# Kernel tuning notes

Hardware: AMD Instinct MI355X
Metric: run time of the kernel (lower is better)

The kernel has to match this reference:

```python
import jax, jax.numpy as jnp
import numpy as np
from jax import lax

B, T = 512, 64
IN, H, V1, P = 256, 512, 101, 8  # input_size, rnn_size, vocab_size+1, max_param
CLS, REG = 512, 512


def setup_inputs() -> dict:
    key = jax.random.key(0)
    ks = jax.random.split(key, 20)
    u = lambda k, s: jax.random.uniform(k, s, jnp.float32, -0.1, 0.1)
    sh = 1.0 / np.sqrt(H)
    ul = lambda k, s: jax.random.uniform(k, s, jnp.float32, -sh, sh)
    return {
        "x": jax.random.normal(ks[0], (B, IN), jnp.float32),
        "y": jax.random.randint(ks[1], (B, T), 0, V1),
        "embed": u(ks[2], (V1, IN)),
        "w_ih0": ul(ks[3], (4 * H, IN)),
        "w_hh0": ul(ks[4], (4 * H, H)),
        "w_ih1": ul(ks[5], (4 * H, H)),
        "w_hh1": ul(ks[6], (4 * H, H)),
        "l1w": u(ks[7], (CLS, H)), "l1b": jnp.zeros((CLS,), jnp.float32),
        "l2w": u(ks[8], (V1, CLS)), "l2b": jnp.zeros((V1,), jnp.float32),
        "r1w": u(ks[9], (REG, H)), "r1b": jnp.zeros((REG,), jnp.float32),
        "r2w": u(ks[10], (V1 * P, V1 + REG)), "r2b": jnp.zeros((V1 * P,), jnp.float32),
    }


def _cell(xi, h, c, wih, whh):
    g = xi @ wih.T + h @ whh.T          # [B, 4H], gate order i,f,g,o (no bias)
    i, f, gg, o = jnp.split(g, 4, axis=-1)
    c = jax.nn.sigmoid(f) * c + jax.nn.sigmoid(i) * jnp.tanh(gg)
    h = jax.nn.sigmoid(o) * jnp.tanh(c)
    return h, c


def reference(x, y, embed, w_ih0, w_hh0, w_ih1, w_hh1,
              l1w, l1b, l2w, l2b, r1w, r1b, r2w, r2b):
    # teacher forcing (sample_prob=0): step-0 input is x, step-i input is embed(y[:, i-1])
    emb = embed[y[:, :-1]]                                  # [B, T-1, IN]
    xt = jnp.concatenate([x[None], jnp.transpose(emb, (1, 0, 2))], axis=0)  # [T, B, IN]

    z = jnp.zeros((x.shape[0], H), x.dtype)

    def step(carry, xi):
        h0, c0, h1, c1 = carry
        h0, c0 = _cell(xi, h0, c0, w_ih0, w_hh0)
        h1, c1 = _cell(h0, h1, c1, w_ih1, w_hh1)
        return (h0, c0, h1, c1), h1

    _, outs = lax.scan(step, (z, z, z, z), xt)              # [T, B, H]

    feat2 = jax.nn.relu(outs @ l1w.T + l1b) @ l2w.T + l2b   # [T, B, V1]
    pgm_score = jax.nn.log_softmax(feat2, axis=-1)
    trans_prob = lax.stop_gradient(jax.nn.softmax(feat2, axis=-1))
    pf1 = jax.nn.relu(outs @ r1w.T + r1b)                   # [T, B, REG]
    ps = (jnp.concatenate([trans_prob, pf1], axis=-1) @ r2w.T + r2b)
    ps = ps.reshape(T, -1, V1, P)                           # [T, B, V1, P]
    idx = y.T                                               # [T, B]
    param = ps[jnp.arange(T)[:, None], jnp.arange(x.shape[0])[None, :], idx]  # [T, B, P]
    return (jnp.transpose(pgm_score, (1, 0, 2)),            # [B, T, V1]
            jnp.transpose(param, (1, 0, 2)))                # [B, T, P]
```

## Files before the change

kernel.cpp:

```cpp
#include <hip/hip_runtime.h>
#include <stdint.h>

typedef unsigned short u16;
typedef short bf16x8 __attribute__((ext_vector_type(8)));
typedef float f32x4 __attribute__((ext_vector_type(4)));
typedef int i32x4 __attribute__((ext_vector_type(4)));

#define DEV static __device__ __forceinline__

constexpr int B_ = 512, T_ = 64, IN_ = 256, H_ = 512, V1_ = 101, P_ = 8, G4_ = 2048;
constexpr int EXR = 613;
constexpr int M_  = T_ * B_;

DEV float b2f(u16 u) { union { uint32_t i; float f; } v; v.i = ((uint32_t)u) << 16; return v.f; }
DEV u16 f2b(float f) {
  union { float f; uint32_t i; } v; v.f = f;
  uint32_t i = v.i;
  return (u16)((i + 0x7fffu + ((i >> 16) & 1u)) >> 16);
}
DEV float sigf(float x) { return 1.f / (1.f + __expf(-x)); }
DEV float tanh_(float x) {
  float c = fminf(fmaxf(x, -15.f), 15.f);
  float e = __expf(2.f * c);
  return (e - 1.f) / (e + 1.f);
}
DEV bf16x8 ld8(const u16* p) { return *reinterpret_cast<const bf16x8*>(p); }
DEV f32x4 mfma16(bf16x8 a, bf16x8 b, f32x4 c) {
  return __builtin_amdgcn_mfma_f32_16x16x32_bf16(a, b, c, 0, 0, 0);
}

struct CvtArgs {
  const float* src[9];
  u16* dst[9];
  int pre[10];
};

__global__ __launch_bounds__(256) void k_cvtall(CvtArgs a) {
  int gid = blockIdx.x * 256 + threadIdx.x;
  if (gid >= a.pre[9]) return;
  int s = 0;
#pragma unroll
  for (int i = 1; i < 9; ++i) s += (gid >= a.pre[i]);
  const int local = gid - a.pre[s];
  const float4 v = reinterpret_cast<const float4*>(a.src[s])[local];
  ushort4 o;
  o.x = f2b(v.x); o.y = f2b(v.y); o.z = f2b(v.z); o.w = f2b(v.w);
  reinterpret_cast<ushort4*>(a.dst[s])[local] = o;
}

__global__ __launch_bounds__(256) void k_precomp(const u16* __restrict__ ex_src,
                                                 const u16* __restrict__ wih0b,
                                                 float* __restrict__ EX0) {
  const int lane = threadIdx.x & 63;
  const int wv = threadIdx.x >> 6;
  const int m0 = blockIdx.x * 64 + wv * 16;
  const int n0 = blockIdx.y * 64;
  const int lr = lane & 15;
  const int lk = (lane >> 4) * 8;

  const int arow = m0 + lr;
  const bool valid = arow < EXR;

  f32x4 acc[4] = {};
  for (int k0 = 0; k0 < IN_; k0 += 32) {
    bf16x8 a = {};
    if (valid) a = ld8(ex_src + (size_t)arow * IN_ + k0 + lk);
#pragma unroll
    for (int c = 0; c < 4; ++c) {
      bf16x8 b = ld8(wih0b + (size_t)(n0 + c * 16 + lr) * IN_ + k0 + lk);
      acc[c] = mfma16(a, b, acc[c]);
    }
  }
  const int rb = (lane >> 4) * 4;
#pragma unroll
  for (int c = 0; c < 4; ++c)
#pragma unroll
    for (int r = 0; r < 4; ++r) {
      int row = m0 + rb + r;
      int col = n0 + c * 16 + (lane & 15);
      if (row < EXR) EX0[(size_t)row * G4_ + col] = acc[c][r];
    }
}

__global__ __launch_bounds__(256, 1) void k_scan(
    const u16* __restrict__ whh0, const u16* __restrict__ wih1, const u16* __restrict__ whh1,
    const float* __restrict__ EX0, const int* __restrict__ y,
    u16* h0buf, u16* h1buf, unsigned* flags ) {
  __shared__ u16 h0s[16 * 512];
  __shared__ u16 h1s[16 * 512];
  __shared__ u16 stg[16][64];
  const size_t BH = (size_t)B_ * H_;
  const int tid = threadIdx.x;
  const int lane = tid & 63;
  const int wv = tid >> 6;
  const int isL1 = blockIdx.x >> 8;
  const int bm = (blockIdx.x >> 3) & 31;
  const int bj = blockIdx.x & 7;
  const int lr = lane & 15;
  const int lk = (lane >> 4) * 8;
  const int col = bj * 64 + wv * 16 + lr;
  const int rb = (lane >> 4) * 4;
  const int lcol = wv * 16 + lr;

  const u16* wpa[4]; const u16* wpb[4];
#pragma unroll
  for (int g = 0; g < 4; ++g) {
    wpa[g] = (isL1 ? wih1 : whh0) + (size_t)(g * H_ + col) * H_ + lk;
    wpb[g] = (isL1 ? whh1 : whh0) + (size_t)(g * H_ + col) * H_ + lk;
  }
  f32x4 cst = {};
  unsigned* gf = flags + bm * 16;
  const int npoll = isL1 ? 16 : 8;

  for (int k = 0; k < T_; ++k) {
    if (wv == 0 && (k > 0 || isL1)) {
      const unsigned thr = (lane < 8) ? (unsigned)(isL1 ? k + 1 : k)
                                      : ((lane < 16 && isL1) ? (unsigned)k : 0u);
      for (;;) {
        unsigned v = 0xffffffffu;
        if (lane < npoll)
          v = __hip_atomic_load(&gf[lane], __ATOMIC_RELAXED, __HIP_MEMORY_SCOPE_AGENT);
        if (__all(v >= thr)) break;
        __builtin_amdgcn_s_sleep(1);
      }
    }
    __syncthreads();

    {
      const u16* h0g = h0buf + (size_t)(k + isL1) * BH + (size_t)(bm * 16) * H_;
#pragma unroll
      for (int rr = 0; rr < 4; ++rr) {
        const int idx = rr * 256 + tid;
        const int row = idx >> 6, cc = idx & 63;
        i32x4 d = *(const i32x4*)(h0g + (size_t)row * H_ + cc * 8);
        *(i32x4*)((char*)h0s + row * 1024 + ((cc * 16) ^ ((row & 7) << 4))) = d;
      }
      if (isL1) {
        const u16* h1g = h1buf + (size_t)k * BH + (size_t)(bm * 16) * H_;
#pragma unroll
        for (int rr = 0; rr < 4; ++rr) {
          const int idx = rr * 256 + tid;
          const int row = idx >> 6, cc = idx & 63;
          i32x4 d = *(const i32x4*)(h1g + (size_t)row * H_ + cc * 8);
          *(i32x4*)((char*)h1s + row * 1024 + ((cc * 16) ^ ((row & 7) << 4))) = d;
        }
      }
    }
    __syncthreads();

    if (!isL1) {
      f32x4 acc[4] = {};
#pragma unroll
      for (int i = 0; i < 16; ++i) {
        bf16x8 a0 = *(const bf16x8*)((const char*)h0s + lr * 1024 + (((i * 32 + lk) * 2) ^ ((lr & 7) << 4)));
#pragma unroll
        for (int g = 0; g < 4; ++g) acc[g] = mfma16(a0, ld8(wpa[g] + i * 32), acc[g]);
      }
#pragma unroll
      for (int r = 0; r < 4; ++r) {
        const int row = bm * 16 + rb + r;
        const int srow = (k == 0) ? (V1_ + row) : y[row * T_ + k - 1];
        const float* bp = EX0 + (size_t)srow * G4_ + col;
        float iv = acc[0][r] + bp[0], fv = acc[1][r] + bp[H_];
        float gv = acc[2][r] + bp[2 * H_], ov = acc[3][r] + bp[3 * H_];
        float cn = sigf(fv) * cst[r] + sigf(iv) * tanh_(gv);
        cst[r] = cn;
        stg[rb + r][lcol] = f2b(sigf(ov) * tanh_(cn));
      }
    } else {
      f32x4 acc[4] = {};
#pragma unroll
      for (int i = 0; i < 16; ++i) {
        const int so = ((i * 32 + lk) * 2) ^ ((lr & 7) << 4);
        bf16x8 a0 = *(const bf16x8*)((const char*)h0s + lr * 1024 + so);
        bf16x8 a1 = *(const bf16x8*)((const char*)h1s + lr * 1024 + so);
#pragma unroll
        for (int g = 0; g < 4; ++g) {
          acc[g] = mfma16(a0, ld8(wpa[g] + i * 32), acc[g]);
          acc[g] = mfma16(a1, ld8(wpb[g] + i * 32), acc[g]);
        }
      }
#pragma unroll
      for (int r = 0; r < 4; ++r) {
        float cn = sigf(acc[1][r]) * cst[r] + sigf(acc[0][r]) * tanh_(acc[2][r]);
        cst[r] = cn;
        stg[rb + r][lcol] = f2b(sigf(acc[3][r]) * tanh_(cn));
      }
    }
    __syncthreads();

    if (tid < 128) {
      const int lrow = tid >> 3, c8 = (tid & 7) * 8;
      i32x4 d = *(const i32x4*)&stg[lrow][c8];
      u16* base = isL1 ? h1buf : h0buf;
      u16* gp = base + (size_t)(k + 1) * BH + (size_t)(bm * 16 + lrow) * H_ + bj * 64 + c8;
      asm volatile("global_store_dwordx4 %0, %1, off sc0 sc1" :: "v"(gp), "v"(d) : "memory");
    }
    asm volatile("s_waitcnt vmcnt(0)" ::: "memory");
    __syncthreads();
    if (tid == 0)
      __hip_atomic_store(&gf[isL1 * 8 + bj], (unsigned)(k + 1),
                         __ATOMIC_RELAXED, __HIP_MEMORY_SCOPE_AGENT);
  }
}

__global__ __launch_bounds__(256) void k_fused1(const u16* __restrict__ outs,
                                                const u16* __restrict__ l1w, const float* __restrict__ l1b,
                                                const u16* __restrict__ r1w, const float* __restrict__ r1b,
                                                u16* __restrict__ feat1, u16* __restrict__ pf1) {
  const int lane = threadIdx.x & 63;
  const int wv = threadIdx.x >> 6;
  const int lr = lane & 15;
  const int lk = (lane >> 4) * 8;
  const int ar = blockIdx.x * 64 + wv * 16 + lr;
  const int rb = (lane >> 4) * 4;
  const int row0 = blockIdx.x * 64 + wv * 16 + rb;

  bf16x8 a[16];
  {
    const u16* ap = outs + (size_t)ar * H_ + lk;
#pragma unroll
    for (int i = 0; i < 16; ++i) a[i] = ld8(ap + i * 32);
  }
  for (int w = 0; w < 2; ++w) {
    const u16* W = w ? r1w : l1w;
    const float* bias = w ? r1b : l1b;
    u16* dst = w ? pf1 : feat1;
    for (int nc = 0; nc < 4; ++nc) {
      f32x4 acc[8] = {};
#pragma unroll
      for (int i = 0; i < 16; ++i)
#pragma unroll
        for (int n = 0; n < 8; ++n)
          acc[n] = mfma16(a[i], ld8(W + (size_t)(nc * 128 + n * 16 + lr) * H_ + i * 32 + lk), acc[n]);
#pragma unroll
      for (int n = 0; n < 8; ++n) {
        const int colc = nc * 128 + n * 16 + lr;
        const float bv = bias[colc];
#pragma unroll
        for (int r = 0; r < 4; ++r)
          dst[(size_t)(row0 + r) * H_ + colc] = f2b(fmaxf(acc[n][r] + bv, 0.f));
      }
    }
  }
}

__global__ __launch_bounds__(256) void k_fused2(const u16* __restrict__ feat1,
                                                const u16* __restrict__ l2w, const float* __restrict__ l2b,
                                                const u16* __restrict__ pf1,
                                                const float* __restrict__ r2w, const float* __restrict__ r2b,
                                                const int* __restrict__ y,
                                                float* __restrict__ pgm, float* __restrict__ par) {
  __shared__ float trans[64][104];
  const int lane = threadIdx.x & 63;
  const int wv = threadIdx.x >> 6;
  const int lr = lane & 15;
  const int lk = (lane >> 4) * 8;
  const int ar = blockIdx.x * 64 + wv * 16 + lr;
  const int rb = (lane >> 4) * 4;

  f32x4 acc[7] = {};
  {
    const u16* ap = feat1 + (size_t)ar * H_ + lk;
#pragma unroll
    for (int i = 0; i < 16; ++i) {
      bf16x8 av = ld8(ap + i * 32);
#pragma unroll
      for (int c = 0; c < 7; ++c) {
        const int n = c * 16 + lr;
        bf16x8 b = {};
        if (n < V1_) b = ld8(l2w + (size_t)n * H_ + i * 32 + lk);
        acc[c] = mfma16(av, b, acc[c]);
      }
    }
  }
#pragma unroll
  for (int r = 0; r < 4; ++r) {
    float v[7];
    float mx = -1e30f;
#pragma unroll
    for (int c = 0; c < 7; ++c) {
      const int colc = c * 16 + lr;
      v[c] = (colc < V1_) ? acc[c][r] + l2b[colc] : -1e30f;
      mx = fmaxf(mx, v[c]);
    }
#pragma unroll
    for (int o = 1; o < 16; o <<= 1) mx = fmaxf(mx, __shfl_xor(mx, o, 64));
    float e[7], s = 0.f;
#pragma unroll
    for (int c = 0; c < 7; ++c) { e[c] = (c * 16 + lr < V1_) ? __expf(v[c] - mx) : 0.f; s += e[c]; }
#pragma unroll
    for (int o = 1; o < 16; o <<= 1) s += __shfl_xor(s, o, 64);
    const float lz = __logf(s), inv = 1.f / s;
    const int m = blockIdx.x * 64 + wv * 16 + rb + r;
    const int t = m >> 9, bb = m & 511;
    float* po = pgm + ((size_t)bb * T_ + t) * V1_;
#pragma unroll
    for (int c = 0; c < 7; ++c) {
      const int colc = c * 16 + lr;
      if (colc < V1_) { po[colc] = v[c] - mx - lz; trans[wv * 16 + rb + r][colc] = e[c] * inv; }
    }
  }
  __syncthreads();
  for (int rr = 0; rr < 16; ++rr) {
    const int m = blockIdx.x * 64 + wv * 16 + rr;
    const int t = m >> 9, bb = m & 511;
    const int idx = y[bb * T_ + t];
    const float* wb = r2w + (size_t)idx * P_ * 613;
    float a8[P_] = {};
    for (int kk = lane; kk < 613; kk += 64) {
      float xv = (kk < V1_) ? trans[wv * 16 + rr][kk] : b2f(pf1[(size_t)m * H_ + kk - V1_]);
#pragma unroll
      for (int p = 0; p < P_; ++p) a8[p] += xv * wb[(size_t)p * 613 + kk];
    }
#pragma unroll
    for (int p = 0; p < P_; ++p)
#pragma unroll
      for (int o = 1; o < 64; o <<= 1) a8[p] += __shfl_xor(a8[p], o, 64);
    if (lane < P_) par[((size_t)bb * T_ + t) * P_ + lane] = a8[lane] + r2b[idx * P_ + lane];
  }
}

extern "C" void kernel_launch(void* const* d_in, const int* in_sizes, int n_in,
                              void* d_out, int out_size, void* d_ws, size_t ws_size,
                              hipStream_t stream) {
  (void)in_sizes; (void)n_in; (void)out_size; (void)ws_size;
  const float* x     = (const float*)d_in[0];
  const int*   y     = (const int*)d_in[1];
  const float* embed = (const float*)d_in[2];
  const float* wih0  = (const float*)d_in[3];
  const float* whh0  = (const float*)d_in[4];
  const float* wih1  = (const float*)d_in[5];
  const float* whh1  = (const float*)d_in[6];
  const float* l1w   = (const float*)d_in[7];
  const float* l1b   = (const float*)d_in[8];
  const float* l2w   = (const float*)d_in[9];
  const float* l2b   = (const float*)d_in[10];
  const float* r1w   = (const float*)d_in[11];
  const float* r1b   = (const float*)d_in[12];
  const float* r2w   = (const float*)d_in[13];
  const float* r2b   = (const float*)d_in[14];

  float* out_pgm = (float*)d_out;
  float* out_par = out_pgm + (size_t)B_ * T_ * V1_;

  char* ws = (char*)d_ws;
  size_t off = 0;
  auto alloc = [&](size_t bytes) { void* p = ws + off; off += (bytes + 255) & ~(size_t)255; return p; };

  const size_t BH2 = (size_t)B_ * H_ * 2;

  unsigned* flags = (unsigned*)alloc(32 * 16 * 4);
  u16* h0buf  = (u16*)alloc((size_t)(T_ + 1) * BH2);
  u16* h1buf  = (u16*)alloc((size_t)(T_ + 1) * BH2);

  float* EX0   = (float*)alloc((size_t)EXR * G4_ * 4);
  u16* ex_src  = (u16*)alloc((size_t)EXR * IN_ * 2);
  u16* wih0b   = (u16*)alloc((size_t)4 * H_ * IN_ * 2);
  u16* whh0b   = (u16*)alloc((size_t)4 * H_ * H_ * 2);
  u16* wih1b   = (u16*)alloc((size_t)4 * H_ * H_ * 2);
  u16* whh1b   = (u16*)alloc((size_t)4 * H_ * H_ * 2);
  u16* l1wb    = (u16*)alloc((size_t)H_ * H_ * 2);
  u16* r1wb    = (u16*)alloc((size_t)H_ * H_ * 2);
  u16* l2wb    = (u16*)alloc((size_t)V1_ * H_ * 2);
  u16* feat1   = (u16*)alloc((size_t)M_ * H_ * 2);
  u16* pf1     = (u16*)alloc((size_t)M_ * H_ * 2);

  (void)hipMemsetAsync(flags, 0, 32 * 16 * 4 + BH2, stream);
  (void)hipMemsetAsync(h1buf, 0, BH2, stream);

  CvtArgs ca;
  const float* srcs[9] = {embed, x, wih0, whh0, wih1, whh1, l1w, r1w, l2w};
  u16* dsts[9] = {ex_src, ex_src + (size_t)V1_ * IN_, wih0b, whh0b, wih1b, whh1b, l1wb, r1wb, l2wb};
  int ns[9] = {V1_ * IN_, B_ * IN_, 4 * H_ * IN_, 4 * H_ * H_, 4 * H_ * H_, 4 * H_ * H_,
               H_ * H_, H_ * H_, V1_ * H_};
  int acc4 = 0;
  for (int i = 0; i < 9; ++i) {
    ca.src[i] = srcs[i]; ca.dst[i] = dsts[i]; ca.pre[i] = acc4; acc4 += ns[i] / 4;
  }
  ca.pre[9] = acc4;
  k_cvtall<<<(acc4 + 255) / 256, 256, 0, stream>>>(ca);

  k_precomp<<<dim3(10, 32), 256, 0, stream>>>(ex_src, wih0b, EX0);

  k_scan<<<512, 256, 0, stream>>>(whh0b, wih1b, whh1b, EX0, y, h0buf, h1buf, flags);

  u16* outs = h1buf + (size_t)B_ * H_;
  k_fused1<<<512, 256, 0, stream>>>(outs, l1wb, l1b, r1wb, r1b, feat1, pf1);
  k_fused2<<<512, 256, 0, stream>>>(feat1, l2wb, l2b, pf1, r2w, r2b, y, out_pgm, out_par);
}
```

Before: 2.089 ms.

## Repartition persistent LSTM scan to 256 blocks of 512 threads, store EX0 in bf16

```diff
diff --git a/kernel.cpp b/kernel.cpp
--- a/kernel.cpp
+++ b/kernel.cpp
@@ -50,7 +50,7 @@
 
 __global__ __launch_bounds__(256) void k_precomp(const u16* __restrict__ ex_src,
                                                  const u16* __restrict__ wih0b,
-                                                 float* __restrict__ EX0) {
+                                                 u16* __restrict__ EX0) {
   const int lane = threadIdx.x & 63;
   const int wv = threadIdx.x >> 6;
   const int m0 = blockIdx.x * 64 + wv * 16;
@@ -78,29 +78,36 @@
     for (int r = 0; r < 4; ++r) {
       int row = m0 + rb + r;
       int col = n0 + c * 16 + (lane & 15);
-      if (row < EXR) EX0[(size_t)row * G4_ + col] = acc[c][r];
-    }
-}
-
-__global__ __launch_bounds__(256, 1) void k_scan(
+      if (row < EXR) EX0[(size_t)row * G4_ + col] = f2b(acc[c][r]);
+    }
+}
+
+__global__ __launch_bounds__(512, 1) void k_scan(
     const u16* __restrict__ whh0, const u16* __restrict__ wih1, const u16* __restrict__ whh1,
-    const float* __restrict__ EX0, const int* __restrict__ y,
+    const u16* __restrict__ EX0, const int* __restrict__ y,
     u16* h0buf, u16* h1buf, unsigned* flags ) {
-  __shared__ u16 h0s[16 * 512];
-  __shared__ u16 h1s[16 * 512];
-  __shared__ u16 stg[16][64];
+  __shared__ u16 h0s[32 * 512];
+  __shared__ u16 h1s[32 * 512];
+  __shared__ u16 stg[2048];
   const size_t BH = (size_t)B_ * H_;
   const int tid = threadIdx.x;
   const int lane = tid & 63;
   const int wv = tid >> 6;
-  const int isL1 = blockIdx.x >> 8;
-  const int bm = (blockIdx.x >> 3) & 31;
-  const int bj = blockIdx.x & 7;
+  const int x_ = blockIdx.x & 7;
+  const int n  = blockIdx.x >> 3;
+  const bool isL1 = x_ >= 4;
+  const int xr = x_ & 3;
+  const int Rb = xr * 128;
   const int lr = lane & 15;
   const int lk = (lane >> 4) * 8;
-  const int col = bj * 64 + wv * 16 + lr;
   const int rb = (lane >> 4) * 4;
-  const int lcol = wv * 16 + lr;
+
+  const int rm = n & 7, cs = n >> 3;
+  const int rm2 = n & 3, cw = n >> 2;
+
+  int col, arow0;
+  if (!isL1) { col = cs * 128 + wv * 16 + lr; arow0 = 0; }
+  else       { col = cw * 64 + (wv >> 1) * 16 + lr; arow0 = (wv & 1) * 16; }
 
   const u16* wpa[4]; const u16* wpb[4];
 #pragma unroll
@@ -109,17 +116,23 @@
     wpb[g] = (isL1 ? whh1 : whh0) + (size_t)(g * H_ + col) * H_ + lk;
   }
   f32x4 cst = {};
-  unsigned* gf = flags + bm * 16;
-  const int npoll = isL1 ? 16 : 8;
+  unsigned* f0g = flags + xr * 32 + (isL1 ? rm2 * 8 : rm * 4);
+  unsigned* f1g = flags + 128 + xr * 32 + rm2 * 8;
+
+  const int row0base = isL1 ? (Rb + rm2 * 32) : (Rb + rm * 16);
+  const int nrows = isL1 ? 32 : 16;
 
   for (int k = 0; k < T_; ++k) {
     if (wv == 0 && (k > 0 || isL1)) {
-      const unsigned thr = (lane < 8) ? (unsigned)(isL1 ? k + 1 : k)
-                                      : ((lane < 16 && isL1) ? (unsigned)k : 0u);
+      unsigned thr = 0; const unsigned* ap = nullptr;
+      if (!isL1) { if (lane < 4) { ap = f0g + lane; thr = (unsigned)k; } }
+      else {
+        if (lane < 8)       { ap = f0g + lane;     thr = (unsigned)(k + 1); }
+        else if (lane < 16) { ap = f1g + lane - 8; thr = (unsigned)k; }
+      }
       for (;;) {
         unsigned v = 0xffffffffu;
-        if (lane < npoll)
-          v = __hip_atomic_load(&gf[lane], __ATOMIC_RELAXED, __HIP_MEMORY_SCOPE_AGENT);
+        if (ap) v = __hip_atomic_load(ap, __ATOMIC_RELAXED, __HIP_MEMORY_SCOPE_AGENT);
         if (__all(v >= thr)) break;
         __builtin_amdgcn_s_sleep(1);
       }
@@ -127,19 +140,16 @@
     __syncthreads();
 
     {
-      const u16* h0g = h0buf + (size_t)(k + isL1) * BH + (size_t)(bm * 16) * H_;
-#pragma unroll
-      for (int rr = 0; rr < 4; ++rr) {
-        const int idx = rr * 256 + tid;
+      const u16* h0g = h0buf + (size_t)(k + (isL1 ? 1 : 0)) * BH + (size_t)row0base * H_;
+      const int nch = nrows * 64;
+      for (int idx = tid; idx < nch; idx += 512) {
         const int row = idx >> 6, cc = idx & 63;
         i32x4 d = *(const i32x4*)(h0g + (size_t)row * H_ + cc * 8);
         *(i32x4*)((char*)h0s + row * 1024 + ((cc * 16) ^ ((row & 7) << 4))) = d;
       }
       if (isL1) {
-        const u16* h1g = h1buf + (size_t)k * BH + (size_t)(bm * 16) * H_;
-#pragma unroll
-        for (int rr = 0; rr < 4; ++rr) {
-          const int idx = rr * 256 + tid;
+        const u16* h1g = h1buf + (size_t)k * BH + (size_t)row0base * H_;
+        for (int idx = tid; idx < nch; idx += 512) {
           const int row = idx >> 6, cc = idx & 63;
           i32x4 d = *(const i32x4*)(h1g + (size_t)row * H_ + cc * 8);
           *(i32x4*)((char*)h1s + row * 1024 + ((cc * 16) ^ ((row & 7) << 4))) = d;
@@ -156,51 +166,60 @@
 #pragma unroll
         for (int g = 0; g < 4; ++g) acc[g] = mfma16(a0, ld8(wpa[g] + i * 32), acc[g]);
       }
+      const int lcol = wv * 16 + lr;
 #pragma unroll
       for (int r = 0; r < 4; ++r) {
-        const int row = bm * 16 + rb + r;
+        const int row = row0base + rb + r;
         const int srow = (k == 0) ? (V1_ + row) : y[row * T_ + k - 1];
-        const float* bp = EX0 + (size_t)srow * G4_ + col;
-        float iv = acc[0][r] + bp[0], fv = acc[1][r] + bp[H_];
-        float gv = acc[2][r] + bp[2 * H_], ov = acc[3][r] + bp[3 * H_];
+        const u16* bp = EX0 + (size_t)srow * G4_ + col;
+        float iv = acc[0][r] + b2f(bp[0]), fv = acc[1][r] + b2f(bp[H_]);
+        float gv = acc[2][r] + b2f(bp[2 * H_]), ov = acc[3][r] + b2f(bp[3 * H_]);
         float cn = sigf(fv) * cst[r] + sigf(iv) * tanh_(gv);
         cst[r] = cn;
-        stg[rb + r][lcol] = f2b(sigf(ov) * tanh_(cn));
+        stg[(rb + r) * 128 + lcol] = f2b(sigf(ov) * tanh_(cn));
       }
     } else {
       f32x4 acc[4] = {};
 #pragma unroll
       for (int i = 0; i < 16; ++i) {
-        const int so = ((i * 32 + lk) * 2) ^ ((lr & 7) << 4);
-        bf16x8 a0 = *(const bf16x8*)((const char*)h0s + lr * 1024 + so);
-        bf16x8 a1 = *(const bf16x8*)((const char*)h1s + lr * 1024 + so);
+        const int so = ((i * 32 + lk) * 2) ^ (((arow0 + lr) & 7) << 4);
+        bf16x8 a0 = *(const bf16x8*)((const char*)h0s + (arow0 + lr) * 1024 + so);
+        bf16x8 a1 = *(const bf16x8*)((const char*)h1s + (arow0 + lr) * 1024 + so);
 #pragma unroll
         for (int g = 0; g < 4; ++g) {
           acc[g] = mfma16(a0, ld8(wpa[g] + i * 32), acc[g]);
           acc[g] = mfma16(a1, ld8(wpb[g] + i * 32), acc[g]);
         }
       }
+      const int lcol = (wv >> 1) * 16 + lr;
 #pragma unroll
       for (int r = 0; r < 4; ++r) {
         float cn = sigf(acc[1][r]) * cst[r] + sigf(acc[0][r]) * tanh_(acc[2][r]);
         cst[r] = cn;
-        stg[rb + r][lcol] = f2b(sigf(acc[3][r]) * tanh_(cn));
+        stg[(arow0 + rb + r) * 64 + lcol] = f2b(sigf(acc[3][r]) * tanh_(cn));
       }
     }
     __syncthreads();
 
-    if (tid < 128) {
-      const int lrow = tid >> 3, c8 = (tid & 7) * 8;
-      i32x4 d = *(const i32x4*)&stg[lrow][c8];
-      u16* base = isL1 ? h1buf : h0buf;
-      u16* gp = base + (size_t)(k + 1) * BH + (size_t)(bm * 16 + lrow) * H_ + bj * 64 + c8;
-      asm volatile("global_store_dwordx4 %0, %1, off sc0 sc1" :: "v"(gp), "v"(d) : "memory");
+    if (tid < 256) {
+      if (!isL1) {
+        const int lrow = tid >> 4, c8 = (tid & 15) * 8;
+        i32x4 d = *(const i32x4*)&stg[lrow * 128 + c8];
+        u16* gp = h0buf + (size_t)(k + 1) * BH + (size_t)(row0base + lrow) * H_ + cs * 128 + c8;
+        asm volatile("global_store_dwordx4 %0, %1, off sc0 sc1" :: "v"(gp), "v"(d) : "memory");
+      } else {
+        const int lrow = tid >> 3, c8 = (tid & 7) * 8;
+        i32x4 d = *(const i32x4*)&stg[lrow * 64 + c8];
+        u16* gp = h1buf + (size_t)(k + 1) * BH + (size_t)(row0base + lrow) * H_ + cw * 64 + c8;
+        asm volatile("global_store_dwordx4 %0, %1, off sc0 sc1" :: "v"(gp), "v"(d) : "memory");
+      }
     }
     asm volatile("s_waitcnt vmcnt(0)" ::: "memory");
     __syncthreads();
-    if (tid == 0)
-      __hip_atomic_store(&gf[isL1 * 8 + bj], (unsigned)(k + 1),
-                         __ATOMIC_RELAXED, __HIP_MEMORY_SCOPE_AGENT);
+    if (tid == 0) {
+      unsigned* fa = isL1 ? &f1g[cw] : &f0g[cs];
+      __hip_atomic_store(fa, (unsigned)(k + 1), __ATOMIC_RELAXED, __HIP_MEMORY_SCOPE_AGENT);
+    }
   }
 }
 
@@ -231,15 +250,15 @@
 #pragma unroll
       for (int i = 0; i < 16; ++i)
 #pragma unroll
-        for (int n = 0; n < 8; ++n)
-          acc[n] = mfma16(a[i], ld8(W + (size_t)(nc * 128 + n * 16 + lr) * H_ + i * 32 + lk), acc[n]);
-#pragma unroll
-      for (int n = 0; n < 8; ++n) {
-        const int colc = nc * 128 + n * 16 + lr;
+        for (int nn = 0; nn < 8; ++nn)
+          acc[nn] = mfma16(a[i], ld8(W + (size_t)(nc * 128 + nn * 16 + lr) * H_ + i * 32 + lk), acc[nn]);
+#pragma unroll
+      for (int nn = 0; nn < 8; ++nn) {
+        const int colc = nc * 128 + nn * 16 + lr;
         const float bv = bias[colc];
 #pragma unroll
         for (int r = 0; r < 4; ++r)
-          dst[(size_t)(row0 + r) * H_ + colc] = f2b(fmaxf(acc[n][r] + bv, 0.f));
+          dst[(size_t)(row0 + r) * H_ + colc] = f2b(fmaxf(acc[nn][r] + bv, 0.f));
       }
     }
   }
@@ -267,9 +286,9 @@
       bf16x8 av = ld8(ap + i * 32);
 #pragma unroll
       for (int c = 0; c < 7; ++c) {
-        const int n = c * 16 + lr;
+        const int nn = c * 16 + lr;
         bf16x8 b = {};
-        if (n < V1_) b = ld8(l2w + (size_t)n * H_ + i * 32 + lk);
+        if (nn < V1_) b = ld8(l2w + (size_t)nn * H_ + i * 32 + lk);
         acc[c] = mfma16(av, b, acc[c]);
       }
     }
@@ -350,11 +369,11 @@
 
   const size_t BH2 = (size_t)B_ * H_ * 2;
 
-  unsigned* flags = (unsigned*)alloc(32 * 16 * 4);
+  unsigned* flags = (unsigned*)alloc(256 * 4);
   u16* h0buf  = (u16*)alloc((size_t)(T_ + 1) * BH2);
   u16* h1buf  = (u16*)alloc((size_t)(T_ + 1) * BH2);
 
-  float* EX0   = (float*)alloc((size_t)EXR * G4_ * 4);
+  u16* EX0b    = (u16*)alloc((size_t)EXR * G4_ * 2);
   u16* ex_src  = (u16*)alloc((size_t)EXR * IN_ * 2);
   u16* wih0b   = (u16*)alloc((size_t)4 * H_ * IN_ * 2);
   u16* whh0b   = (u16*)alloc((size_t)4 * H_ * H_ * 2);
@@ -366,7 +385,7 @@
   u16* feat1   = (u16*)alloc((size_t)M_ * H_ * 2);
   u16* pf1     = (u16*)alloc((size_t)M_ * H_ * 2);
 
-  (void)hipMemsetAsync(flags, 0, 32 * 16 * 4 + BH2, stream);
+  (void)hipMemsetAsync(flags, 0, 256 * 4 + BH2, stream);
   (void)hipMemsetAsync(h1buf, 0, BH2, stream);
 
   CvtArgs ca;
@@ -381,9 +400,9 @@
   ca.pre[9] = acc4;
   k_cvtall<<<(acc4 + 255) / 256, 256, 0, stream>>>(ca);
 
-  k_precomp<<<dim3(10, 32), 256, 0, stream>>>(ex_src, wih0b, EX0);
-
-  k_scan<<<512, 256, 0, stream>>>(whh0b, wih1b, whh1b, EX0, y, h0buf, h1buf, flags);
+  k_precomp<<<dim3(10, 32), 256, 0, stream>>>(ex_src, wih0b, EX0b);
+
+  k_scan<<<256, 512, 0, stream>>>(whh0b, wih1b, whh1b, EX0b, y, h0buf, h1buf, flags);
 
   u16* outs = h1buf + (size_t)B_ * H_;
   k_fused1<<<512, 256, 0, stream>>>(outs, l1wb, l1b, r1wb, r1b, feat1, pf1);
```

Measured after the change: 2.448 ms. +17.2%, slower.
